# Optimization experiments

Measured on AMD Instinct MI355X. Metric: run time of the kernel, lower is better.

Reference implementation:

```python
import jax, jax.numpy as jnp
import numpy as np

B = 16      # number of point clouds
N = 4096    # points per cloud (max after densify)
D = 3       # xyz


def setup_inputs() -> dict:
    key = jax.random.key(0)
    k1, k2 = jax.random.split(key)
    pred = jax.random.normal(k1, (B * N, D), dtype=jnp.float32)
    target = jax.random.normal(k2, (B * N, D), dtype=jnp.float32)
    # sorted segment ids, equal-sized clouds (faithful to to_dense_batch usage)
    batch = jnp.repeat(jnp.arange(B, dtype=jnp.int64), N)
    return {"pred": pred, "target": target, "batch": batch}


def to_dense_batch(x, batch, num_batches, max_n):
    # PyG to_dense_batch: scatter flat points into [B, max_n, D], zero-padded.
    ones = jnp.ones_like(batch)
    counts = jax.ops.segment_sum(ones, batch, num_segments=num_batches)
    offsets = jnp.concatenate([jnp.zeros((1,), batch.dtype), jnp.cumsum(counts)[:-1]])
    pos = jnp.arange(batch.shape[0], dtype=batch.dtype) - offsets[batch]
    dense = jnp.zeros((num_batches, max_n, x.shape[-1]), x.dtype)
    return dense.at[batch, pos].set(x)


def chamfer_distance(x, y):
    # squared-euclidean pairwise distances via the GEMM identity
    x2 = jnp.sum(x * x, axis=-1)                      # [B, N]
    y2 = jnp.sum(y * y, axis=-1)                      # [B, M]
    xy = jnp.einsum('bnd,bmd->bnm', x, y)             # [B, N, M]
    d = x2[:, :, None] + y2[:, None, :] - 2.0 * xy    # [B, N, M]
    cham_x = jnp.mean(jnp.min(d, axis=2), axis=1)     # mean over N of min over M
    cham_y = jnp.mean(jnp.min(d, axis=1), axis=1)     # mean over M of min over N
    # point_reduction='mean', batch_reduction='mean' (pytorch3d defaults)
    return jnp.mean(cham_x + cham_y)


def reference(pred, target, batch):
    x = to_dense_batch(pred, batch, B, N)
    y = to_dense_batch(target, batch, B, N)
    return chamfer_distance(x, y)
```

## Files before the change

kernel.cpp:

```cpp
#include <hip/hip_runtime.h>


namespace {

constexpr int kB = 16;
constexpr int kN = 4096;
constexpr int kPlane = kB * kN;
constexpr int kQ = 4;
constexpr int kQL = kN / kQ;
constexpr float kScale = 1.0f / (float)(kB * kN);

typedef short bf16x8 __attribute__((ext_vector_type(8)));
typedef float f32x16 __attribute__((ext_vector_type(16)));
typedef unsigned short u16;

__device__ inline u16 bf16_rn(float f) {
  union { float f; unsigned u; } v; v.f = f;
  unsigned r = v.u + 0x7fffu + ((v.u >> 16) & 1u);
  return (u16)(r >> 16);
}
__device__ inline float bf16_f(u16 h) {
  union { unsigned u; float f; } v; v.u = (unsigned)h << 16;
  return v.f;
}
__device__ inline unsigned pk2(u16 lo, u16 hi) {
  return (unsigned)lo | ((unsigned)hi << 16);
}

__global__ void init_out(float* out) { out[0] = 0.0f; }

__global__ __launch_bounds__(256) void cd_prep(
    const float* __restrict__ pred, const float* __restrict__ targ,
    u16* __restrict__ Ab, u16* __restrict__ Bb, float* __restrict__ out) {
  const int p = blockIdx.x * 256 + threadIdx.x;
  if (p == 0) out[0] = 0.0f;
  const u16 one = 0x3F80;
  {
    const float a = pred[3 * p], c = pred[3 * p + 1], d = pred[3 * p + 2];
    const u16 ah = bf16_rn(a), ch = bf16_rn(c), dh = bf16_rn(d);
    const u16 al = bf16_rn(a - bf16_f(ah));
    const u16 cl = bf16_rn(c - bf16_f(ch));
    const u16 dl = bf16_rn(d - bf16_f(dh));
    const float s2 = fmaf(a, a, fmaf(c, c, d * d));
    const u16 s2h = bf16_rn(s2);
    const u16 s2l = bf16_rn(s2 - bf16_f(s2h));
    uint4 w0, w1;
    w0.x = pk2(ah, ch); w0.y = pk2(dh, al); w0.z = pk2(cl, dl); w0.w = pk2(ah, ch);
    w1.x = pk2(dh, s2h); w1.y = pk2(s2l, one); w1.z = pk2(one, al); w1.w = pk2(cl, dl);
    uint4* dst = reinterpret_cast<uint4*>(Ab + (size_t)p * 16);
    dst[0] = w0; dst[1] = w1;
  }
  {
    const float a = targ[3 * p], c = targ[3 * p + 1], d = targ[3 * p + 2];
    const u16 ah0 = bf16_rn(a), ch0 = bf16_rn(c), dh0 = bf16_rn(d);
    const u16 ah = bf16_rn(-2.0f * bf16_f(ah0));
    const u16 ch = bf16_rn(-2.0f * bf16_f(ch0));
    const u16 dh = bf16_rn(-2.0f * bf16_f(dh0));
    const u16 al = bf16_rn(-2.0f * bf16_f(bf16_rn(a - bf16_f(ah0))));
    const u16 cl = bf16_rn(-2.0f * bf16_f(bf16_rn(c - bf16_f(ch0))));
    const u16 dl = bf16_rn(-2.0f * bf16_f(bf16_rn(d - bf16_f(dh0))));
    const float s2 = fmaf(a, a, fmaf(c, c, d * d));
    const u16 s2h = bf16_rn(s2);
    const u16 s2l = bf16_rn(s2 - bf16_f(s2h));
    uint4 w0, w1;
    w0.x = pk2(ah, ch); w0.y = pk2(dh, ah); w0.z = pk2(ch, dh); w0.w = pk2(al, cl);
    w1.x = pk2(dl, one); w1.y = pk2(one, s2h); w1.z = pk2(s2l, al); w1.w = pk2(cl, dl);
    uint4* dst = reinterpret_cast<uint4*>(Bb + (size_t)p * 16);
    dst[0] = w0; dst[1] = w1;
  }
}

__global__ __launch_bounds__(256) void cd_rowmin(
    const u16* __restrict__ Ab, const u16* __restrict__ Bb,
    float* __restrict__ rowpart) {
  const int t = threadIdx.x;
  const int w = t >> 6, lane = t & 63;
  const int half = lane >> 5, l31 = lane & 31;
  const int chunk = blockIdx.x;
  const int cloud = blockIdx.y;
  const int dir = blockIdx.z;

  const u16* __restrict__ RowM = dir ? Bb : Ab;
  const u16* __restrict__ ColM = dir ? Ab : Bb;

  bf16x8 af[4];
#pragma unroll
  for (int a = 0; a < 4; ++a) {
    const int arow = cloud * kN + chunk * 128 + a * 32 + l31;
    af[a] = *(const bf16x8*)(RowM + (size_t)arow * 16 + half * 8);
  }

  f32x16 zacc;
#pragma unroll
  for (int r = 0; r < 16; ++r) zacc[r] = 0.0f;
  float rmin[4][16];
#pragma unroll
  for (int a = 0; a < 4; ++a)
#pragma unroll
    for (int r = 0; r < 16; ++r) rmin[a][r] = 1e30f;

  const u16* bbase = ColM + ((size_t)cloud * kN + w * kQL) * 16;
  constexpr int NT = kQL / 64;
  const int jcol = l31 * 16 + half * 8;
  for (int jt = 0; jt < NT; ++jt) {
    const u16* bp = bbase + jt * 64 * 16;
    const bf16x8 b0 = *(const bf16x8*)(bp + jcol);
    const bf16x8 b1 = *(const bf16x8*)(bp + 32 * 16 + jcol);
#pragma unroll
    for (int a = 0; a < 4; ++a) {
      const f32x16 s0 =
          __builtin_amdgcn_mfma_f32_32x32x16_bf16(af[a], b0, zacc, 0, 0, 0);
      const f32x16 s1 =
          __builtin_amdgcn_mfma_f32_32x32x16_bf16(af[a], b1, zacc, 0, 0, 0);
#pragma unroll
      for (int r = 0; r < 16; ++r)
        rmin[a][r] = fminf(rmin[a][r], fminf(s0[r], s1[r]));
    }
  }

#pragma unroll
  for (int st = 1; st < 32; st <<= 1) {
#pragma unroll
    for (int a = 0; a < 4; ++a)
#pragma unroll
      for (int r = 0; r < 16; ++r)
        rmin[a][r] = fminf(rmin[a][r], __shfl_xor(rmin[a][r], st, 64));
  }
  if (l31 == 0) {
    float* rp =
        rowpart + (((size_t)dir * kQ + w) * kB + cloud) * kN + chunk * 128;
#pragma unroll
    for (int a = 0; a < 4; ++a)
#pragma unroll
      for (int r = 0; r < 16; ++r) {
        const int row = (r & 3) + 8 * (r >> 2) + 4 * half;
        rp[a * 32 + row] = rmin[a][r];
      }
  }
}

__global__ __launch_bounds__(256) void cd_reduce(
    const float* __restrict__ rowpart, float* __restrict__ out) {
  const int u = blockIdx.x * 256 + threadIdx.x;
  const int dir = u >> 16, rest = u & (kPlane - 1);
  const int cloud = rest >> 12, p = rest & (kN - 1);
  float rm = 1e30f;
#pragma unroll
  for (int q = 0; q < kQ; ++q)
    rm = fminf(rm, rowpart[(((size_t)dir * kQ + q) * kB + cloud) * kN + p]);
  float s = rm;
  for (int o = 32; o > 0; o >>= 1) s += __shfl_down(s, o, 64);
  __shared__ float wsum[4];
  const int lane = threadIdx.x & 63, wv = threadIdx.x >> 6;
  if (lane == 0) wsum[wv] = s;
  __syncthreads();
  if (threadIdx.x == 0)
    atomicAdd(out, (wsum[0] + wsum[1] + wsum[2] + wsum[3]) * kScale);
}

template <int KX>
__global__ __launch_bounds__(256) void chamfer_direct(
    const float* __restrict__ pred, const float* __restrict__ targ,
    float* __restrict__ out) {
  __shared__ float4 tA[128], tB[128];
  const int t = threadIdx.x;
  const int xb = blockIdx.x, b = blockIdx.y, dir = blockIdx.z;
  const float* __restrict__ X = dir ? targ : pred;
  const float* __restrict__ Y = dir ? pred : targ;
  float2 xx2[KX], xy2[KX], xz2[KX];
  float x2[KX], mn[KX];
  const int ibase = b * kN + xb * (256 * KX) + t;
#pragma unroll
  for (int k = 0; k < KX; ++k) {
    const int i = ibase + k * 256;
    const float a = X[3 * i], c = X[3 * i + 1], d = X[3 * i + 2];
    x2[k] = fmaf(a, a, fmaf(c, c, d * d));
    xx2[k] = make_float2(-2.0f * a, -2.0f * a);
    xy2[k] = make_float2(-2.0f * c, -2.0f * c);
    xz2[k] = make_float2(-2.0f * d, -2.0f * d);
    mn[k] = 1e30f;
  }
  for (int t0 = 0; t0 < kN; t0 += 256) {
    __syncthreads();
    if (t < 128) {
      const int j0 = 3 * (b * kN + t0 + 2 * t);
      const float a0 = Y[j0], c0 = Y[j0 + 1], d0 = Y[j0 + 2];
      const float a1 = Y[j0 + 3], c1 = Y[j0 + 4], d1 = Y[j0 + 5];
      tA[t] = make_float4(a0, a1, c0, c1);
      tB[t] = make_float4(d0, d1, fmaf(a0, a0, fmaf(c0, c0, d0 * d0)),
                          fmaf(a1, a1, fmaf(c1, c1, d1 * d1)));
    }
    __syncthreads();
    for (int jj = 0; jj < 128; ++jj) {
      const float4 qa = tA[jj], qb = tB[jj];
      const float2 qx = make_float2(qa.x, qa.y), qy = make_float2(qa.z, qa.w);
      const float2 qz = make_float2(qb.x, qb.y), qw = make_float2(qb.z, qb.w);
#pragma unroll
      for (int k = 0; k < KX; ++k) {
        float2 acc;
        asm("v_pk_fma_f32 %0, %1, %2, %3\n\t"
            "v_pk_fma_f32 %0, %4, %5, %0\n\t"
            "v_pk_fma_f32 %0, %6, %7, %0"
            : "=&v"(acc)
            : "v"(xz2[k]), "v"(qz), "v"(qw), "v"(xy2[k]), "v"(qy),
              "v"(xx2[k]), "v"(qx));
        asm("v_min3_f32 %0, %0, %1, %2" : "+v"(mn[k]) : "v"(acc.x), "v"(acc.y));
      }
    }
  }
  float s = 0.0f;
#pragma unroll
  for (int k = 0; k < KX; ++k) s += x2[k] + mn[k];
  for (int o = 32; o > 0; o >>= 1) s += __shfl_down(s, o, 64);
  __shared__ float wsum[4];
  const int lane = t & 63, wv = t >> 6;
  if (lane == 0) wsum[wv] = s;
  __syncthreads();
  if (t == 0)
    atomicAdd(out, (wsum[0] + wsum[1] + wsum[2] + wsum[3]) * kScale);
}

}

extern "C" void kernel_launch(void* const* d_in, const int* in_sizes, int n_in,
                              void* d_out, int out_size, void* d_ws,
                              size_t ws_size, hipStream_t stream) {
  const float* pred = (const float*)d_in[0];
  const float* targ = (const float*)d_in[1];
  float* out = (float*)d_out;

  const size_t needA = (size_t)kPlane * 16 * sizeof(u16);
  const size_t needRow = (size_t)2 * kQ * kPlane * sizeof(float);
  if (ws_size >= 2 * needA + needRow) {
    u16* Ab = (u16*)d_ws;
    u16* Bb = (u16*)((char*)d_ws + needA);
    float* rowpart = (float*)((char*)d_ws + 2 * needA);
    cd_prep<<<dim3(kPlane / 256), 256, 0, stream>>>(pred, targ, Ab, Bb, out);
    cd_rowmin<<<dim3(32, kB, 2), 256, 0, stream>>>(Ab, Bb, rowpart);
    cd_reduce<<<dim3(2 * kPlane / 256), 256, 0, stream>>>(rowpart, out);
  } else {
    init_out<<<dim3(1), dim3(1), 0, stream>>>(out);
    constexpr int KX = 8;
    dim3 grid(kN / (256 * KX), kB, 2);
    chamfer_direct<KX><<<grid, 256, 0, stream>>>(pred, targ, out);
  }
}
```

Measured before the change: 112.0 us.

## Stage column tiles in LDS and split column range across blocks

After: 114.8 us. +2.5%, slower.

```diff
diff --git a/kernel.cpp b/kernel.cpp
--- a/kernel.cpp
+++ b/kernel.cpp
@@ -6,8 +6,8 @@
 constexpr int kB = 16;
 constexpr int kN = 4096;
 constexpr int kPlane = kB * kN;
-constexpr int kQ = 4;
-constexpr int kQL = kN / kQ;
+constexpr int kJS = 2;
+constexpr int kJSL = kN / kJS;
 constexpr float kScale = 1.0f / (float)(kB * kN);
 
 typedef short bf16x8 __attribute__((ext_vector_type(8)));
@@ -73,64 +73,80 @@
 __global__ __launch_bounds__(256) void cd_rowmin(
     const u16* __restrict__ Ab, const u16* __restrict__ Bb,
     float* __restrict__ rowpart) {
+  __shared__ u16 tile[256 * 16];
+
   const int t = threadIdx.x;
   const int w = t >> 6, lane = t & 63;
   const int half = lane >> 5, l31 = lane & 31;
   const int chunk = blockIdx.x;
   const int cloud = blockIdx.y;
-  const int dir = blockIdx.z;
+  const int z = blockIdx.z;
+  const int dir = z >> 1;
+  const int slice = z & 1;
 
   const u16* __restrict__ RowM = dir ? Bb : Ab;
   const u16* __restrict__ ColM = dir ? Ab : Bb;
 
-  bf16x8 af[4];
-#pragma unroll
-  for (int a = 0; a < 4; ++a) {
-    const int arow = cloud * kN + chunk * 128 + a * 32 + l31;
+  bf16x8 af[2];
+#pragma unroll
+  for (int a = 0; a < 2; ++a) {
+    const int arow = cloud * kN + chunk * 256 + w * 64 + a * 32 + l31;
     af[a] = *(const bf16x8*)(RowM + (size_t)arow * 16 + half * 8);
   }
 
   f32x16 zacc;
 #pragma unroll
   for (int r = 0; r < 16; ++r) zacc[r] = 0.0f;
-  float rmin[4][16];
-#pragma unroll
-  for (int a = 0; a < 4; ++a)
+  float rmin[2][16];
+#pragma unroll
+  for (int a = 0; a < 2; ++a)
 #pragma unroll
     for (int r = 0; r < 16; ++r) rmin[a][r] = 1e30f;
 
-  const u16* bbase = ColM + ((size_t)cloud * kN + w * kQL) * 16;
-  constexpr int NT = kQL / 64;
+  const u16* bslice = ColM + ((size_t)cloud * kN + slice * kJSL) * 16;
   const int jcol = l31 * 16 + half * 8;
-  for (int jt = 0; jt < NT; ++jt) {
-    const u16* bp = bbase + jt * 64 * 16;
-    const bf16x8 b0 = *(const bf16x8*)(bp + jcol);
-    const bf16x8 b1 = *(const bf16x8*)(bp + 32 * 16 + jcol);
-#pragma unroll
-    for (int a = 0; a < 4; ++a) {
-      const f32x16 s0 =
-          __builtin_amdgcn_mfma_f32_32x32x16_bf16(af[a], b0, zacc, 0, 0, 0);
-      const f32x16 s1 =
-          __builtin_amdgcn_mfma_f32_32x32x16_bf16(af[a], b1, zacc, 0, 0, 0);
-#pragma unroll
-      for (int r = 0; r < 16; ++r)
-        rmin[a][r] = fminf(rmin[a][r], fminf(s0[r], s1[r]));
+  constexpr int NTILE = kJSL / 256;
+
+  for (int tb = 0; tb < NTILE; ++tb) {
+    __syncthreads();
+    {
+      const uint4* s4 = (const uint4*)(bslice + (size_t)tb * 256 * 16);
+      uint4* d4 = (uint4*)tile;
+      d4[t] = s4[t];
+      d4[256 + t] = s4[256 + t];
+    }
+    __syncthreads();
+#pragma unroll
+    for (int g = 0; g < 4; ++g) {
+      const u16* lp = tile + g * 64 * 16;
+      const bf16x8 b0 = *(const bf16x8*)(lp + jcol);
+      const bf16x8 b1 = *(const bf16x8*)(lp + 32 * 16 + jcol);
+#pragma unroll
+      for (int a = 0; a < 2; ++a) {
+        const f32x16 s0 =
+            __builtin_amdgcn_mfma_f32_32x32x16_bf16(af[a], b0, zacc, 0, 0, 0);
+        const f32x16 s1 =
+            __builtin_amdgcn_mfma_f32_32x32x16_bf16(af[a], b1, zacc, 0, 0, 0);
+#pragma unroll
+        for (int r = 0; r < 16; ++r)
+          rmin[a][r] = fminf(rmin[a][r], fminf(s0[r], s1[r]));
+      }
     }
   }
 
 #pragma unroll
   for (int st = 1; st < 32; st <<= 1) {
 #pragma unroll
-    for (int a = 0; a < 4; ++a)
+    for (int a = 0; a < 2; ++a)
 #pragma unroll
       for (int r = 0; r < 16; ++r)
         rmin[a][r] = fminf(rmin[a][r], __shfl_xor(rmin[a][r], st, 64));
   }
   if (l31 == 0) {
     float* rp =
-        rowpart + (((size_t)dir * kQ + w) * kB + cloud) * kN + chunk * 128;
-#pragma unroll
-    for (int a = 0; a < 4; ++a)
+        rowpart + ((size_t)z * kB + cloud) * kN + chunk * 256 + w * 64;
+#pragma unroll
+    for (int a = 0; a < 2; ++a)
 #pragma unroll
       for (int r = 0; r < 16; ++r) {
         const int row = (r & 3) + 8 * (r >> 2) + 4 * half;
@@ -146,8 +162,8 @@
   const int cloud = rest >> 12, p = rest & (kN - 1);
   float rm = 1e30f;
 #pragma unroll
-  for (int q = 0; q < kQ; ++q)
-    rm = fminf(rm, rowpart[(((size_t)dir * kQ + q) * kB + cloud) * kN + p]);
+  for (int s2 = 0; s2 < kJS; ++s2)
+    rm = fminf(rm, rowpart[(((size_t)(dir * kJS + s2)) * kB + cloud) * kN + p]);
   float s = rm;
   for (int o = 32; o > 0; o >>= 1) s += __shfl_down(s, o, 64);
   __shared__ float wsum[4];
@@ -230,13 +246,13 @@
   float* out = (float*)d_out;
 
   const size_t needA = (size_t)kPlane * 16 * sizeof(u16);
-  const size_t needRow = (size_t)2 * kQ * kPlane * sizeof(float);
+  const size_t needRow = (size_t)2 * kJS * kPlane * sizeof(float);
   if (ws_size >= 2 * needA + needRow) {
     u16* Ab = (u16*)d_ws;
     u16* Bb = (u16*)((char*)d_ws + needA);
     float* rowpart = (float*)((char*)d_ws + 2 * needA);
     cd_prep<<<dim3(kPlane / 256), 256, 0, stream>>>(pred, targ, Ab, Bb, out);
-    cd_rowmin<<<dim3(32, kB, 2), 256, 0, stream>>>(Ab, Bb, rowpart);
+    cd_rowmin<<<dim3(16, kB, 2 * kJS), 256, 0, stream>>>(Ab, Bb, rowpart);
     cd_reduce<<<dim3(2 * kPlane / 256), 256, 0, stream>>>(rowpart, out);
   } else {
     init_out<<<dim3(1), dim3(1), 0, stream>>>(out);
```
